# Kernel optimization log

Hardware: AMD Instinct MI355X
Metric: run time of the kernel (lower is better)

Reference implementation:

```python
import jax, jax.numpy as jnp
import numpy as np
import math

E = 1024   # embed_dim
H = 16     # num_heads
D = E // H # head_dim


def _rotary(x):
    # x: [B, H, S, D]. Faithful to the original quirky implementation:
    # pos_enc[:, 0::2] = sin(position * div_term), then cos/sin are taken OF that value.
    S = x.shape[2]
    position = jnp.arange(S, dtype=jnp.float32)[:, None]                     # [S,1]
    div_term = jnp.exp(jnp.arange(0, D, 2, dtype=jnp.float32) * (-math.log(10000.0) / D))  # [D/2]
    angle = jnp.sin(position * div_term)                                     # [S, D/2] == pos_enc[:,0::2]
    cos_t = jnp.cos(angle)                                                   # [S, D/2]
    sin_t = jnp.sin(angle)                                                   # [S, D/2]
    xe = x[..., 0::2]
    xo = x[..., 1::2]
    re = xe * cos_t - xo * sin_t
    ro = xo * cos_t + xe * sin_t
    # interleave even/odd back: [..., D/2, 2] -> [..., D]
    return jnp.stack([re, ro], axis=-1).reshape(x.shape)


def setup_inputs() -> dict:
    key = jax.random.key(0)
    ks = jax.random.split(key, 12)
    B, S = 4, 1024
    scale = 1.0 / math.sqrt(E)
    inp = {
        "query": jax.random.normal(ks[0], (B, S, E), dtype=jnp.float32),
        "key":   jax.random.normal(ks[1], (B, S, E), dtype=jnp.float32),
        "value": jax.random.normal(ks[2], (B, S, E), dtype=jnp.float32),
        # Linear params stored as [in, out]; y = x @ W + b
        "Wq": jax.random.normal(ks[3], (E, E), dtype=jnp.float32) * scale,
        "bq": jnp.zeros((E,), dtype=jnp.float32),
        "Wk": jax.random.normal(ks[4], (E, E), dtype=jnp.float32) * scale,
        "bk": jnp.zeros((E,), dtype=jnp.float32),
        "Wv": jax.random.normal(ks[5], (E, E), dtype=jnp.float32) * scale,
        "bv": jnp.zeros((E,), dtype=jnp.float32),
        "Wo": jax.random.normal(ks[6], (E, E), dtype=jnp.float32) * scale,
        "bo": jnp.zeros((E,), dtype=jnp.float32),
    }
    return inp


def reference(query, key, value, Wq, bq, Wk, bk, Wv, bv, Wo, bo):
    B, S, _ = query.shape
    # projections -> [B, H, S, D]
    q = (query @ Wq + bq).reshape(B, S, H, D).transpose(0, 2, 1, 3)
    k = (key   @ Wk + bk).reshape(B, S, H, D).transpose(0, 2, 1, 3)
    v = (value @ Wv + bv).reshape(B, S, H, D).transpose(0, 2, 1, 3)
    q = _rotary(q)
    k = _rotary(k)
    scores = jnp.einsum('bhsd,bhtd->bhst', q, k) / (D ** 0.5)  # [B,H,S,S]
    probs = jax.nn.softmax(scores, axis=-1)
    # dropout p=0 (eval) -> identity
    ctx = jnp.einsum('bhst,bhtd->bhsd', probs, v)              # [B,H,S,D]
    ctx = ctx.transpose(0, 2, 1, 3).reshape(B, S, E)
    out = ctx @ Wo + bo
    return out, probs
```

## Files before the change

kernel.cpp:

```cpp
#include <hip/hip_runtime.h>
#include <hip/hip_bf16.h>

typedef __attribute__((ext_vector_type(8))) short bf16x8;
typedef __attribute__((ext_vector_type(4))) float f32x4;
typedef unsigned short u16;

__device__ __forceinline__ u16 f2bf(float f) {
  unsigned u = __float_as_uint(f);
  u += 0x7fffu + ((u >> 16) & 1u);
  return (u16)(u >> 16);
}

__device__ __forceinline__ void gload16(const void* g, void* l) {
  __builtin_amdgcn_global_load_lds(
      (const __attribute__((address_space(1))) unsigned int*)g,
      (__attribute__((address_space(3))) unsigned int*)l, 16, 0, 0);
}

__device__ __forceinline__ void blockbar() {
  asm volatile("" ::: "memory");
  __builtin_amdgcn_s_barrier();
  asm volatile("" ::: "memory");
}

__global__ __launch_bounds__(256) void prep_kernel(
    const float* __restrict__ query, const float* __restrict__ key_,
    const float* __restrict__ value, u16* __restrict__ qin,
    u16* __restrict__ kin, u16* __restrict__ vin,
    const float* __restrict__ Wq, const float* __restrict__ Wk,
    const float* __restrict__ Wv, const float* __restrict__ Wo,
    u16* __restrict__ WqT, u16* __restrict__ WkT, u16* __restrict__ WvT,
    u16* __restrict__ WoT, float* __restrict__ cosT, float* __restrict__ sinT) {
  __shared__ float tile[32][33];
  const int z = blockIdx.z;
  const int bx = blockIdx.x;
  const int tid = threadIdx.x;
  if (z < 3) {
    const float* in = z == 0 ? query : z == 1 ? key_ : value;
    u16* out = z == 0 ? qin : z == 1 ? kin : vin;
    size_t i = ((size_t)bx * 256 + tid) * 4;
    float4 v = *(const float4*)(in + i);
    ushort4 o = make_ushort4(f2bf(v.x), f2bf(v.y), f2bf(v.z), f2bf(v.w));
    *(ushort4*)(out + i) = o;
  } else if (z == 3) {
    const int w = bx >> 10;
    const float* W = w == 0 ? Wq : w == 1 ? Wk : w == 2 ? Wv : Wo;
    u16* Wt = w == 0 ? WqT : w == 1 ? WkT : w == 2 ? WvT : WoT;
    int tx = tid & 31, ty = tid >> 5;
    int k0 = ((bx >> 5) & 31) * 32, n0 = (bx & 31) * 32;
#pragma unroll
    for (int i = 0; i < 4; ++i)
      tile[ty + i * 8][tx] = W[(size_t)(k0 + ty + i * 8) * 1024 + n0 + tx];
    __syncthreads();
#pragma unroll
    for (int i = 0; i < 4; ++i)
      Wt[(size_t)(n0 + ty + i * 8) * 1024 + k0 + tx] = f2bf(tile[tx][ty + i * 8]);
  } else {
    int i = bx * 256 + tid;
    if (i >= 1024 * 32) return;
    int s = i >> 5, p = i & 31;
    double freq = exp(-9.210340371976184 * (double)(2 * p) / 64.0);
    double ang = sin((double)s * freq);
    cosT[i] = (float)cos(ang);
    sinT[i] = (float)sin(ang);
  }
}

__global__ __launch_bounds__(256) void proj_gemm_kernel(
    const u16* __restrict__ qin, const u16* __restrict__ kin,
    const u16* __restrict__ vin, const u16* __restrict__ WqT,
    const u16* __restrict__ WkT, const u16* __restrict__ WvT,
    const float* __restrict__ bq, const float* __restrict__ bk,
    const float* __restrict__ bv, u16* __restrict__ qr, u16* __restrict__ kr,
    u16* __restrict__ vt, const float* __restrict__ cosT,
    const float* __restrict__ sinT) {
  __shared__ u16 lA[2][128 * 32];
  __shared__ u16 lB[2][128 * 32];
  const int z = blockIdx.z;
  const u16* A = z == 0 ? qin : z == 1 ? kin : vin;
  const u16* Bt = z == 0 ? WqT : z == 1 ? WkT : WvT;
  const float* bias = z == 0 ? bq : z == 1 ? bk : bv;

  const int tid = threadIdx.x;
  const int lane = tid & 63, wid = tid >> 6;
  const int wm = wid >> 1, wn = wid & 1;
  const int lr = lane & 15, kg = lane >> 4;
  const int m0 = blockIdx.y * 128, n0 = blockIdx.x * 128;

  auto stage = [&](int bu, int k0) {
#pragma unroll
    for (int it = 0; it < 2; ++it) {
      int o = tid * 16 + it * 4096;
      int row = o >> 6;
      int cbs = (((o >> 4) & 3) ^ (row & 3)) << 4;
      gload16((const char*)A + ((size_t)(m0 + row) * 1024 + k0) * 2 + cbs,
              (char*)lA[bu] + o);
      gload16((const char*)Bt + ((size_t)(n0 + row) * 1024 + k0) * 2 + cbs,
              (char*)lB[bu] + o);
    }
  };

  stage(0, 0);
  f32x4 acc[4][4] = {};
  for (int t = 0; t < 32; ++t) {
    if (t < 31) {
      stage((t + 1) & 1, (t + 1) * 32);
      asm volatile("s_waitcnt vmcnt(4)" ::: "memory");
    } else {
      asm volatile("s_waitcnt vmcnt(0)" ::: "memory");
    }
    blockbar();
    const int cb = t & 1;
    bf16x8 av[4], bv_[4];
#pragma unroll
    for (int i = 0; i < 4; ++i) {
      int ra = wm * 64 + i * 16 + lr;
      av[i] = *(const bf16x8*)((const char*)lA[cb] + ra * 64 + ((kg ^ (ra & 3)) << 4));
      int rb = wn * 64 + i * 16 + lr;
      bv_[i] = *(const bf16x8*)((const char*)lB[cb] + rb * 64 + ((kg ^ (rb & 3)) << 4));
    }
#pragma unroll
    for (int i = 0; i < 4; ++i)
#pragma unroll
      for (int j = 0; j < 4; ++j)
        acc[i][j] = __builtin_amdgcn_mfma_f32_16x16x32_bf16(av[i], bv_[j], acc[i][j], 0, 0, 0);
    blockbar();
  }

  if (z == 2) {
    const int bb = m0 >> 10;
#pragma unroll
    for (int i = 0; i < 4; ++i) {
      int srow = (m0 & 1023) + wm * 64 + i * 16 + kg * 4;
#pragma unroll
      for (int j = 0; j < 4; ++j) {
        int col = n0 + wn * 64 + j * 16 + lr;
        float bcol = bias[col];
        int h = col >> 6, d = col & 63;
        ushort4 o;
        o.x = f2bf(acc[i][j][0] + bcol);
        o.y = f2bf(acc[i][j][1] + bcol);
        o.z = f2bf(acc[i][j][2] + bcol);
        o.w = f2bf(acc[i][j][3] + bcol);
        *(ushort4*)(vt + ((size_t)((bb * 16 + h) * 64 + d)) * 1024 + srow) = o;
      }
    }
  } else {
    u16* Cout = z == 0 ? qr : kr;
#pragma unroll
    for (int i = 0; i < 4; ++i) {
#pragma unroll
      for (int j = 0; j < 4; ++j) {
        int col = n0 + wn * 64 + j * 16 + lr;
        float bcol = bias[col];
#pragma unroll
        for (int r = 0; r < 4; ++r) {
          int row = m0 + wm * 64 + i * 16 + kg * 4 + r;
          float v = acc[i][j][r] + bcol;
          float pv = __shfl_xor(v, 1);
          int p = (col & 63) >> 1;
          int s = row & 1023;
          float ct = cosT[s * 32 + p], st = sinT[s * 32 + p];
          float ov = (col & 1) ? (v * ct + pv * st) : (v * ct - pv * st);
          Cout[(size_t)row * 1024 + col] = f2bf(ov);
        }
      }
    }
  }
}

__global__ __launch_bounds__(256) void out_gemm_kernel(
    const u16* __restrict__ A, const u16* __restrict__ Bt,
    const float* __restrict__ bias, float* __restrict__ Cout) {
  __shared__ u16 lA[2][128 * 32];
  __shared__ u16 lB[2][128 * 32];
  const int tid = threadIdx.x;
  const int lane = tid & 63, wid = tid >> 6;
  const int wm = wid >> 1, wn = wid & 1;
  const int lr = lane & 15, kg = lane >> 4;
  const int m0 = blockIdx.y * 128, n0 = blockIdx.x * 128;

  auto stage = [&](int bu, int k0) {
#pragma unroll
    for (int it = 0; it < 2; ++it) {
      int o = tid * 16 + it * 4096;
      int row = o >> 6;
      int cbs = (((o >> 4) & 3) ^ (row & 3)) << 4;
      gload16((const char*)A + ((size_t)(m0 + row) * 1024 + k0) * 2 + cbs,
              (char*)lA[bu] + o);
      gload16((const char*)Bt + ((size_t)(n0 + row) * 1024 + k0) * 2 + cbs,
              (char*)lB[bu] + o);
    }
  };

  stage(0, 0);
  f32x4 acc[4][4] = {};
  for (int t = 0; t < 32; ++t) {
    if (t < 31) {
      stage((t + 1) & 1, (t + 1) * 32);
      asm volatile("s_waitcnt vmcnt(4)" ::: "memory");
    } else {
      asm volatile("s_waitcnt vmcnt(0)" ::: "memory");
    }
    blockbar();
    const int cb = t & 1;
    bf16x8 av[4], bv_[4];
#pragma unroll
    for (int i = 0; i < 4; ++i) {
      int ra = wm * 64 + i * 16 + lr;
      av[i] = *(const bf16x8*)((const char*)lA[cb] + ra * 64 + ((kg ^ (ra & 3)) << 4));
      int rb = wn * 64 + i * 16 + lr;
      bv_[i] = *(const bf16x8*)((const char*)lB[cb] + rb * 64 + ((kg ^ (rb & 3)) << 4));
    }
#pragma unroll
    for (int i = 0; i < 4; ++i)
#pragma unroll
      for (int j = 0; j < 4; ++j)
        acc[i][j] = __builtin_amdgcn_mfma_f32_16x16x32_bf16(av[i], bv_[j], acc[i][j], 0, 0, 0);
    blockbar();
  }
#pragma unroll
  for (int i = 0; i < 4; ++i)
#pragma unroll
    for (int j = 0; j < 4; ++j) {
      int col = n0 + wn * 64 + j * 16 + lr;
      float bcol = bias[col];
#pragma unroll
      for (int r = 0; r < 4; ++r) {
        int row = m0 + wm * 64 + i * 16 + kg * 4 + r;
        Cout[(size_t)row * 1024 + col] = acc[i][j][r] + bcol;
      }
    }
}

__global__ __launch_bounds__(256, 2) void fused_attn_kernel(
    const u16* __restrict__ qr, const u16* __restrict__ kr,
    const u16* __restrict__ vt, float* __restrict__ probs,
    u16* __restrict__ ctx) {
  __shared__ u16 lQ[32 * 64];
  __shared__ u16 lK[2][128 * 64];
  __shared__ u16 lV[2][64 * 128];
  __shared__ u16 lP[32 * 128];
  __shared__ float redM[4][32];
  __shared__ float redS[4][32];

  const int tid = threadIdx.x;
  const int lane = tid & 63, wid = tid >> 6;
  const int lr = lane & 15, kg = lane >> 4;
  const int z = blockIdx.y, b = z >> 4, h = z & 15;
  const int m0 = blockIdx.x * 32;

  const char* Qb = (const char*)qr + ((size_t)(b * 1024 + m0) * 1024 + h * 64) * 2;
  const char* Kb = (const char*)kr + ((size_t)(b * 1024) * 1024 + h * 64) * 2;
  const char* Vb = (const char*)vt + (size_t)z * 64 * 1024 * 2;

  auto stageK = [&](int bu, int c) {
#pragma unroll
    for (int it = 0; it < 4; ++it) {
      int o = tid * 16 + it * 4096;
      int row = o >> 7, ch = (o >> 4) & 7;
      gload16(Kb + (size_t)(c * 128 + row) * 2048 + ((ch ^ (row & 7)) << 4),
              (char*)lK[bu] + o);
    }
  };
  auto stageV = [&](int bu, int c) {
#pragma unroll
    for (int it = 0; it < 4; ++it) {
      int o = tid * 16 + it * 4096;
      int row = o >> 8, ch = (o >> 4) & 15;
      gload16(Vb + (size_t)row * 2048 + c * 256 + ((ch ^ (row & 15)) << 4),
              (char*)lV[bu] + o);
    }
  };

  {
    int o = tid * 16;
    int row = o >> 7, ch = (o >> 4) & 7;
    gload16(Qb + (size_t)row * 2048 + ((ch ^ (row & 7)) << 4), (char*)lQ + o);
  }
  stageK(0, 0);

  bf16x8 qf[2][2];
  f32x4 accS[8][2][2] = {};
#pragma unroll
  for (int c = 0; c < 8; ++c) {
    if (c < 7) {
      stageK((c + 1) & 1, c + 1);
      asm volatile("s_waitcnt vmcnt(4)" ::: "memory");
    } else {
      asm volatile("s_waitcnt vmcnt(0)" ::: "memory");
    }
    blockbar();
    if (c == 0) {
#pragma unroll
      for (int ii = 0; ii < 2; ++ii)
#pragma unroll
        for (int ks = 0; ks < 2; ++ks) {
          int ra = ii * 16 + lr;
          int cc = ks * 4 + kg;
          qf[ii][ks] = *(const bf16x8*)((const char*)lQ + ra * 128 + ((cc ^ (ra & 7)) << 4));
        }
    }
#pragma unroll
    for (int ks = 0; ks < 2; ++ks) {
      bf16x8 bvf[2];
#pragma unroll
      for (int jj = 0; jj < 2; ++jj) {
        int rb = wid * 32 + jj * 16 + lr;
        int cc = ks * 4 + kg;
        bvf[jj] = *(const bf16x8*)((const char*)lK[c & 1] + rb * 128 + ((cc ^ (rb & 7)) << 4));
      }
#pragma unroll
      for (int ii = 0; ii < 2; ++ii)
#pragma unroll
        for (int jj = 0; jj < 2; ++jj)
          accS[c][ii][jj] =
              __builtin_amdgcn_mfma_f32_16x16x32_bf16(qf[ii][ks], bvf[jj], accS[c][ii][jj], 0, 0, 0);
    }
    blockbar();
  }

  stageV(0, 0);

  float rmax[2][4];
#pragma unroll
  for (int ii = 0; ii < 2; ++ii)
#pragma unroll
    for (int r = 0; r < 4; ++r) rmax[ii][r] = -1e30f;
#pragma unroll
  for (int c = 0; c < 8; ++c)
#pragma unroll
    for (int ii = 0; ii < 2; ++ii)
#pragma unroll
      for (int jj = 0; jj < 2; ++jj)
#pragma unroll
        for (int r = 0; r < 4; ++r) {
          float v = accS[c][ii][jj][r] * 0.125f;
          accS[c][ii][jj][r] = v;
          rmax[ii][r] = fmaxf(rmax[ii][r], v);
        }
#pragma unroll
  for (int ii = 0; ii < 2; ++ii)
#pragma unroll
    for (int r = 0; r < 4; ++r) {
      float v = rmax[ii][r];
      v = fmaxf(v, __shfl_xor(v, 1));
      v = fmaxf(v, __shfl_xor(v, 2));
      v = fmaxf(v, __shfl_xor(v, 4));
      v = fmaxf(v, __shfl_xor(v, 8));
      rmax[ii][r] = v;
    }
  if (lr == 0) {
#pragma unroll
    for (int ii = 0; ii < 2; ++ii)
#pragma unroll
      for (int r = 0; r < 4; ++r) redM[wid][ii * 16 + kg * 4 + r] = rmax[ii][r];
  }
  asm volatile("s_waitcnt lgkmcnt(0)" ::: "memory");
  blockbar();
  float rowm[2][4], rsum[2][4];
#pragma unroll
  for (int ii = 0; ii < 2; ++ii)
#pragma unroll
    for (int r = 0; r < 4; ++r) {
      int row = ii * 16 + kg * 4 + r;
      rowm[ii][r] = fmaxf(fmaxf(redM[0][row], redM[1][row]), fmaxf(redM[2][row], redM[3][row]));
      rsum[ii][r] = 0.f;
    }
#pragma unroll
  for (int c = 0; c < 8; ++c)
#pragma unroll
    for (int ii = 0; ii < 2; ++ii)
#pragma unroll
      for (int jj = 0; jj < 2; ++jj)
#pragma unroll
        for (int r = 0; r < 4; ++r) {
          float e = __expf(accS[c][ii][jj][r] - rowm[ii][r]);
          accS[c][ii][jj][r] = e;
          rsum[ii][r] += e;
        }
#pragma unroll
  for (int ii = 0; ii < 2; ++ii)
#pragma unroll
    for (int r = 0; r < 4; ++r) {
      float v = rsum[ii][r];
      v += __shfl_xor(v, 1);
      v += __shfl_xor(v, 2);
      v += __shfl_xor(v, 4);
      v += __shfl_xor(v, 8);
      rsum[ii][r] = v;
    }
  if (lr == 0) {
#pragma unroll
    for (int ii = 0; ii < 2; ++ii)
#pragma unroll
      for (int r = 0; r < 4; ++r) redS[wid][ii * 16 + kg * 4 + r] = rsum[ii][r];
  }
  asm volatile("s_waitcnt lgkmcnt(0)" ::: "memory");
  blockbar();
  float inv[2][4];
#pragma unroll
  for (int ii = 0; ii < 2; ++ii)
#pragma unroll
    for (int r = 0; r < 4; ++r) {
      int row = ii * 16 + kg * 4 + r;
      inv[ii][r] = 1.0f / (redS[0][row] + redS[1][row] + redS[2][row] + redS[3][row]);
    }

  const int ipv = wid >> 1, jpv = wid & 1;
  f32x4 accPV[2] = {};
  float* Pg = probs + (size_t)z * 1024 * 1024 + (size_t)m0 * 1024;

#pragma unroll
  for (int c = 0; c < 8; ++c) {
    if (c < 7) stageV((c + 1) & 1, c + 1);
#pragma unroll
    for (int ii = 0; ii < 2; ++ii)
#pragma unroll
      for (int jj = 0; jj < 2; ++jj)
#pragma unroll
        for (int r = 0; r < 4; ++r) {
          float p = accS[c][ii][jj][r] * inv[ii][r];
          int row = ii * 16 + kg * 4 + r;
          int col = wid * 32 + jj * 16 + lr;
          Pg[(size_t)row * 1024 + c * 128 + col] = p;
          *(u16*)((char*)lP + row * 256 + ((((col >> 3) ^ (row & 15))) << 4) + (col & 7) * 2) =
              f2bf(p);
        }
    if (c < 7)
      asm volatile("s_waitcnt vmcnt(20) lgkmcnt(0)" ::: "memory");
    else
      asm volatile("s_waitcnt vmcnt(16) lgkmcnt(0)" ::: "memory");
    blockbar();
#pragma unroll
    for (int ks = 0; ks < 4; ++ks) {
      int cc = ks * 4 + kg;
      int ra = ipv * 16 + lr;
      bf16x8 pa = *(const bf16x8*)((const char*)lP + ra * 256 + ((cc ^ (ra & 15)) << 4));
#pragma unroll
      for (int jjj = 0; jjj < 2; ++jjj) {
        int rb = jpv * 32 + jjj * 16 + lr;
        bf16x8 vbf = *(const bf16x8*)((const char*)lV[c & 1] + rb * 256 + ((cc ^ (rb & 15)) << 4));
        accPV[jjj] = __builtin_amdgcn_mfma_f32_16x16x32_bf16(pa, vbf, accPV[jjj], 0, 0, 0);
      }
    }
    blockbar();
  }

#pragma unroll
  for (int jjj = 0; jjj < 2; ++jjj)
#pragma unroll
    for (int r = 0; r < 4; ++r) {
      int row = m0 + ipv * 16 + kg * 4 + r;
      int d = jpv * 32 + jjj * 16 + lr;
      ctx[((size_t)(b * 1024 + row)) * 1024 + h * 64 + d] = f2bf(accPV[jjj][r]);
    }
}

extern "C" void kernel_launch(void* const* d_in, const int* in_sizes, int n_in,
                              void* d_out, int out_size, void* d_ws, size_t ws_size,
                              hipStream_t stream) {
  const float* query = (const float*)d_in[0];
  const float* key_ = (const float*)d_in[1];
  const float* value = (const float*)d_in[2];
  const float* Wq = (const float*)d_in[3];
  const float* bq = (const float*)d_in[4];
  const float* Wk = (const float*)d_in[5];
  const float* bk = (const float*)d_in[6];
  const float* Wv = (const float*)d_in[7];
  const float* bv = (const float*)d_in[8];
  const float* Wo = (const float*)d_in[9];
  const float* bo = (const float*)d_in[10];

  float* out = (float*)d_out;
  float* probs = out + (size_t)4 * 1024 * 1024;

  char* w = (char*)d_ws;
  const size_t SZ_MK = (size_t)4096 * 1024 * 2;
  const size_t SZ_W = (size_t)1024 * 1024 * 2;
  u16* qin = (u16*)w; w += SZ_MK;
  u16* kin = (u16*)w; w += SZ_MK;
  u16* vin = (u16*)w; w += SZ_MK;
  u16* qr = (u16*)w; w += SZ_MK;
  u16* kr = (u16*)w; w += SZ_MK;
  u16* vt = (u16*)w; w += SZ_MK;
  u16* WqT = (u16*)w; w += SZ_W;
  u16* WkT = (u16*)w; w += SZ_W;
  u16* WvT = (u16*)w; w += SZ_W;
  u16* WoT = (u16*)w; w += SZ_W;
  float* cosT = (float*)w; w += 1024 * 32 * 4;
  float* sinT = (float*)w; w += 1024 * 32 * 4;
  u16* ctx = qin;

  dim3 blk(256);
  hipLaunchKernelGGL(prep_kernel, dim3(4096, 1, 5), blk, 0, stream,
                     query, key_, value, qin, kin, vin, Wq, Wk, Wv, Wo,
                     WqT, WkT, WvT, WoT, cosT, sinT);
  hipLaunchKernelGGL(proj_gemm_kernel, dim3(8, 32, 3), blk, 0, stream,
                     qin, kin, vin, WqT, WkT, WvT, bq, bk, bv, qr, kr, vt,
                     cosT, sinT);
  hipLaunchKernelGGL(fused_attn_kernel, dim3(32, 64), blk, 0, stream,
                     qr, kr, vt, probs, ctx);
  hipLaunchKernelGGL(out_gemm_kernel, dim3(8, 32), blk, 0, stream,
                     ctx, WoT, bo, out);
}
```

Baseline: 189.1 us.

## Recompute QK^T in two-pass softmax to cut registers and LDS for occupancy

The attention kernel no longer keeps all 8 score chunks in registers. A first pass computes QK^T only to accumulate exp row sums. A second pass over 64-column chunks recomputes the scores, normalises them, writes probs as float4, and does P·V, with K and V staged together in a shared double buffer. Max subtraction is dropped and operands are swapped so each lane holds contiguous columns. Together with the smaller LDS footprint, this lets launch bounds rise to 4 blocks per CU, at the cost of doing the QK^T MFMAs twice and risking exp overflow when score magnitudes are large.

```diff
diff --git a/kernel.cpp b/kernel.cpp
--- a/kernel.cpp
+++ b/kernel.cpp
@@ -233,15 +233,12 @@
     }
 }
 
-__global__ __launch_bounds__(256, 2) void fused_attn_kernel(
+__global__ __launch_bounds__(256, 4) void fused_attn_kernel(
     const u16* __restrict__ qr, const u16* __restrict__ kr,
     const u16* __restrict__ vt, float* __restrict__ probs,
     u16* __restrict__ ctx) {
-  __shared__ u16 lQ[32 * 64];
-  __shared__ u16 lK[2][128 * 64];
-  __shared__ u16 lV[2][64 * 128];
-  __shared__ u16 lP[32 * 128];
-  __shared__ float redM[4][32];
+  __shared__ u16 big[2][8192];
+  __shared__ u16 lP[32 * 64];
   __shared__ float redS[4][32];
 
   const int tid = threadIdx.x;
@@ -254,196 +251,148 @@
   const char* Kb = (const char*)kr + ((size_t)(b * 1024) * 1024 + h * 64) * 2;
   const char* Vb = (const char*)vt + (size_t)z * 64 * 1024 * 2;
 
-  auto stageK = [&](int bu, int c) {
+  bf16x8 qf[2][2];
+#pragma unroll
+  for (int ii = 0; ii < 2; ++ii)
+#pragma unroll
+    for (int ks = 0; ks < 2; ++ks)
+      qf[ii][ks] =
+          *(const bf16x8*)(Qb + (size_t)(ii * 16 + lr) * 2048 + (ks * 4 + kg) * 16);
+
+  auto stage1 = [&](int bu, int c) {
 #pragma unroll
     for (int it = 0; it < 4; ++it) {
       int o = tid * 16 + it * 4096;
       int row = o >> 7, ch = (o >> 4) & 7;
       gload16(Kb + (size_t)(c * 128 + row) * 2048 + ((ch ^ (row & 7)) << 4),
-              (char*)lK[bu] + o);
+              (char*)big[bu] + o);
     }
   };
-  auto stageV = [&](int bu, int c) {
-#pragma unroll
-    for (int it = 0; it < 4; ++it) {
+  auto stage2 = [&](int bu, int c2) {
+#pragma unroll
+    for (int it = 0; it < 2; ++it) {
       int o = tid * 16 + it * 4096;
-      int row = o >> 8, ch = (o >> 4) & 15;
-      gload16(Vb + (size_t)row * 2048 + c * 256 + ((ch ^ (row & 15)) << 4),
-              (char*)lV[bu] + o);
+      int row = o >> 7, ch = (o >> 4) & 7;
+      gload16(Kb + (size_t)(c2 * 64 + row) * 2048 + ((ch ^ (row & 7)) << 4),
+              (char*)big[bu] + o);
+    }
+#pragma unroll
+    for (int it = 0; it < 2; ++it) {
+      int o = tid * 16 + it * 4096;
+      int row = o >> 7, ch = (o >> 4) & 7;
+      gload16(Vb + (size_t)row * 2048 + c2 * 128 + ((ch ^ (row & 7)) << 4),
+              (char*)big[bu] + 8192 + o);
     }
   };
 
-  {
-    int o = tid * 16;
-    int row = o >> 7, ch = (o >> 4) & 7;
-    gload16(Qb + (size_t)row * 2048 + ((ch ^ (row & 7)) << 4), (char*)lQ + o);
-  }
-  stageK(0, 0);
-
-  bf16x8 qf[2][2];
-  f32x4 accS[8][2][2] = {};
-#pragma unroll
+  float rsum[2] = {0.f, 0.f};
+  stage1(0, 0);
+#pragma unroll 2
   for (int c = 0; c < 8; ++c) {
     if (c < 7) {
-      stageK((c + 1) & 1, c + 1);
+      stage1((c + 1) & 1, c + 1);
       asm volatile("s_waitcnt vmcnt(4)" ::: "memory");
     } else {
       asm volatile("s_waitcnt vmcnt(0)" ::: "memory");
     }
     blockbar();
-    if (c == 0) {
-#pragma unroll
-      for (int ii = 0; ii < 2; ++ii)
-#pragma unroll
-        for (int ks = 0; ks < 2; ++ks) {
-          int ra = ii * 16 + lr;
-          int cc = ks * 4 + kg;
-          qf[ii][ks] = *(const bf16x8*)((const char*)lQ + ra * 128 + ((cc ^ (ra & 7)) << 4));
-        }
-    }
+    const char* KB = (const char*)big[c & 1];
+    f32x4 aS[2][2] = {};
 #pragma unroll
     for (int ks = 0; ks < 2; ++ks) {
-      bf16x8 bvf[2];
+      bf16x8 kf[2];
 #pragma unroll
       for (int jj = 0; jj < 2; ++jj) {
         int rb = wid * 32 + jj * 16 + lr;
-        int cc = ks * 4 + kg;
-        bvf[jj] = *(const bf16x8*)((const char*)lK[c & 1] + rb * 128 + ((cc ^ (rb & 7)) << 4));
+        kf[jj] = *(const bf16x8*)(KB + rb * 128 + (((ks * 4 + kg) ^ (rb & 7)) << 4));
       }
 #pragma unroll
       for (int ii = 0; ii < 2; ++ii)
 #pragma unroll
         for (int jj = 0; jj < 2; ++jj)
-          accS[c][ii][jj] =
-              __builtin_amdgcn_mfma_f32_16x16x32_bf16(qf[ii][ks], bvf[jj], accS[c][ii][jj], 0, 0, 0);
-    }
-    blockbar();
-  }
-
-  stageV(0, 0);
-
-  float rmax[2][4];
-#pragma unroll
-  for (int ii = 0; ii < 2; ++ii)
-#pragma unroll
-    for (int r = 0; r < 4; ++r) rmax[ii][r] = -1e30f;
-#pragma unroll
-  for (int c = 0; c < 8; ++c)
+          aS[ii][jj] =
+              __builtin_amdgcn_mfma_f32_16x16x32_bf16(kf[jj], qf[ii][ks], aS[ii][jj], 0, 0, 0);
+    }
 #pragma unroll
     for (int ii = 0; ii < 2; ++ii)
 #pragma unroll
       for (int jj = 0; jj < 2; ++jj)
 #pragma unroll
-        for (int r = 0; r < 4; ++r) {
-          float v = accS[c][ii][jj][r] * 0.125f;
-          accS[c][ii][jj][r] = v;
-          rmax[ii][r] = fmaxf(rmax[ii][r], v);
-        }
-#pragma unroll
-  for (int ii = 0; ii < 2; ++ii)
-#pragma unroll
-    for (int r = 0; r < 4; ++r) {
-      float v = rmax[ii][r];
-      v = fmaxf(v, __shfl_xor(v, 1));
-      v = fmaxf(v, __shfl_xor(v, 2));
-      v = fmaxf(v, __shfl_xor(v, 4));
-      v = fmaxf(v, __shfl_xor(v, 8));
-      rmax[ii][r] = v;
-    }
-  if (lr == 0) {
-#pragma unroll
-    for (int ii = 0; ii < 2; ++ii)
-#pragma unroll
-      for (int r = 0; r < 4; ++r) redM[wid][ii * 16 + kg * 4 + r] = rmax[ii][r];
-  }
-  asm volatile("s_waitcnt lgkmcnt(0)" ::: "memory");
+        for (int r = 0; r < 4; ++r)
+          rsum[ii] += __expf(aS[ii][jj][r] * 0.125f);
+    blockbar();
+  }
+
+  stage2(0, 0);
+
+#pragma unroll
+  for (int ii = 0; ii < 2; ++ii) {
+    float v = rsum[ii];
+    v += __shfl_xor(v, 16);
+    v += __shfl_xor(v, 32);
+    rsum[ii] = v;
+  }
+  if (lane < 16) {
+    redS[wid][lane] = rsum[0];
+    redS[wid][16 + lane] = rsum[1];
+  }
+  asm volatile("s_waitcnt vmcnt(0) lgkmcnt(0)" ::: "memory");
   blockbar();
-  float rowm[2][4], rsum[2][4];
-#pragma unroll
-  for (int ii = 0; ii < 2; ++ii)
-#pragma unroll
-    for (int r = 0; r < 4; ++r) {
-      int row = ii * 16 + kg * 4 + r;
-      rowm[ii][r] = fmaxf(fmaxf(redM[0][row], redM[1][row]), fmaxf(redM[2][row], redM[3][row]));
-      rsum[ii][r] = 0.f;
-    }
-#pragma unroll
-  for (int c = 0; c < 8; ++c)
-#pragma unroll
-    for (int ii = 0; ii < 2; ++ii)
-#pragma unroll
-      for (int jj = 0; jj < 2; ++jj)
-#pragma unroll
-        for (int r = 0; r < 4; ++r) {
-          float e = __expf(accS[c][ii][jj][r] - rowm[ii][r]);
-          accS[c][ii][jj][r] = e;
-          rsum[ii][r] += e;
-        }
-#pragma unroll
-  for (int ii = 0; ii < 2; ++ii)
-#pragma unroll
-    for (int r = 0; r < 4; ++r) {
-      float v = rsum[ii][r];
-      v += __shfl_xor(v, 1);
-      v += __shfl_xor(v, 2);
-      v += __shfl_xor(v, 4);
-      v += __shfl_xor(v, 8);
-      rsum[ii][r] = v;
-    }
-  if (lr == 0) {
-#pragma unroll
-    for (int ii = 0; ii < 2; ++ii)
-#pragma unroll
-      for (int r = 0; r < 4; ++r) redS[wid][ii * 16 + kg * 4 + r] = rsum[ii][r];
-  }
-  asm volatile("s_waitcnt lgkmcnt(0)" ::: "memory");
-  blockbar();
-  float inv[2][4];
-#pragma unroll
-  for (int ii = 0; ii < 2; ++ii)
-#pragma unroll
-    for (int r = 0; r < 4; ++r) {
-      int row = ii * 16 + kg * 4 + r;
-      inv[ii][r] = 1.0f / (redS[0][row] + redS[1][row] + redS[2][row] + redS[3][row]);
-    }
+  float inv[2];
+#pragma unroll
+  for (int ii = 0; ii < 2; ++ii) {
+    int row = ii * 16 + lr;
+    inv[ii] = 1.0f / (redS[0][row] + redS[1][row] + redS[2][row] + redS[3][row]);
+  }
 
   const int ipv = wid >> 1, jpv = wid & 1;
   f32x4 accPV[2] = {};
   float* Pg = probs + (size_t)z * 1024 * 1024 + (size_t)m0 * 1024;
 
-#pragma unroll
-  for (int c = 0; c < 8; ++c) {
-    if (c < 7) stageV((c + 1) & 1, c + 1);
-#pragma unroll
-    for (int ii = 0; ii < 2; ++ii)
-#pragma unroll
-      for (int jj = 0; jj < 2; ++jj)
-#pragma unroll
-        for (int r = 0; r < 4; ++r) {
-          float p = accS[c][ii][jj][r] * inv[ii][r];
-          int row = ii * 16 + kg * 4 + r;
-          int col = wid * 32 + jj * 16 + lr;
-          Pg[(size_t)row * 1024 + c * 128 + col] = p;
-          *(u16*)((char*)lP + row * 256 + ((((col >> 3) ^ (row & 15))) << 4) + (col & 7) * 2) =
-              f2bf(p);
-        }
-    if (c < 7)
-      asm volatile("s_waitcnt vmcnt(20) lgkmcnt(0)" ::: "memory");
-    else
-      asm volatile("s_waitcnt vmcnt(16) lgkmcnt(0)" ::: "memory");
-    blockbar();
-#pragma unroll
-    for (int ks = 0; ks < 4; ++ks) {
-      int cc = ks * 4 + kg;
+#pragma unroll 2
+  for (int c2 = 0; c2 < 16; ++c2) {
+    const int cur = c2 & 1;
+    if (c2 < 15) stage2(cur ^ 1, c2 + 1);
+    const char* KB = (const char*)big[cur];
+    f32x4 aS2[2] = {};
+#pragma unroll
+    for (int ks = 0; ks < 2; ++ks) {
+      int rb = wid * 16 + lr;
+      bf16x8 kf = *(const bf16x8*)(KB + rb * 128 + (((ks * 4 + kg) ^ (rb & 7)) << 4));
+#pragma unroll
+      for (int ii = 0; ii < 2; ++ii)
+        aS2[ii] = __builtin_amdgcn_mfma_f32_16x16x32_bf16(kf, qf[ii][ks], aS2[ii], 0, 0, 0);
+    }
+#pragma unroll
+    for (int ii = 0; ii < 2; ++ii) {
+      float4 p4;
+      p4.x = __expf(aS2[ii][0] * 0.125f) * inv[ii];
+      p4.y = __expf(aS2[ii][1] * 0.125f) * inv[ii];
+      p4.z = __expf(aS2[ii][2] * 0.125f) * inv[ii];
+      p4.w = __expf(aS2[ii][3] * 0.125f) * inv[ii];
+      int row = ii * 16 + lr;
+      *(float4*)(Pg + (size_t)row * 1024 + c2 * 64 + wid * 16 + kg * 4) = p4;
+      int bytecol = (wid * 16 + kg * 4) * 2;
+      int ch = bytecol >> 4, sub = bytecol & 15;
+      ushort4 pb = make_ushort4(f2bf(p4.x), f2bf(p4.y), f2bf(p4.z), f2bf(p4.w));
+      *(ushort4*)((char*)lP + row * 128 + ((ch ^ (row & 7)) << 4) + sub) = pb;
+    }
+    asm volatile("s_waitcnt lgkmcnt(0)" ::: "memory");
+    blockbar();
+    const char* VB = (const char*)big[cur] + 8192;
+#pragma unroll
+    for (int ks = 0; ks < 2; ++ks) {
       int ra = ipv * 16 + lr;
-      bf16x8 pa = *(const bf16x8*)((const char*)lP + ra * 256 + ((cc ^ (ra & 15)) << 4));
+      bf16x8 pa =
+          *(const bf16x8*)((const char*)lP + ra * 128 + (((ks * 4 + kg) ^ (ra & 7)) << 4));
 #pragma unroll
       for (int jjj = 0; jjj < 2; ++jjj) {
         int rb = jpv * 32 + jjj * 16 + lr;
-        bf16x8 vbf = *(const bf16x8*)((const char*)lV[c & 1] + rb * 256 + ((cc ^ (rb & 15)) << 4));
+        bf16x8 vbf = *(const bf16x8*)(VB + rb * 128 + (((ks * 4 + kg) ^ (rb & 7)) << 4));
         accPV[jjj] = __builtin_amdgcn_mfma_f32_16x16x32_bf16(pa, vbf, accPV[jjj], 0, 0, 0);
       }
     }
+    if (c2 < 15) asm volatile("s_waitcnt vmcnt(2)" ::: "memory");
     blockbar();
   }
 
```

New measurement: 197.3 us. 4.3% more time.

## Split fused attention work across eight waves per block

Applied to the files above, without the earlier changes.

Raises the fused attention block from 256 to 512 threads. Each wave now owns 16 key columns instead of 32 in QK^T and a single 16x16 output tile in PV, which halves the per-thread score accumulator registers. Staging loads, waitcnt thresholds and the cross-wave max/sum reductions are rescaled for eight waves. The aim is more waves in flight to hide latency, at the cost of more barrier participants and less fragment reuse per wave.

```diff
diff --git a/kernel.cpp b/kernel.cpp
--- a/kernel.cpp
+++ b/kernel.cpp
@@ -233,7 +233,7 @@
     }
 }
 
-__global__ __launch_bounds__(256, 2) void fused_attn_kernel(
+__global__ __launch_bounds__(512, 4) void fused_attn_kernel(
     const u16* __restrict__ qr, const u16* __restrict__ kr,
     const u16* __restrict__ vt, float* __restrict__ probs,
     u16* __restrict__ ctx) {
@@ -241,8 +241,8 @@
   __shared__ u16 lK[2][128 * 64];
   __shared__ u16 lV[2][64 * 128];
   __shared__ u16 lP[32 * 128];
-  __shared__ float redM[4][32];
-  __shared__ float redS[4][32];
+  __shared__ float redM[8][32];
+  __shared__ float redS[8][32];
 
   const int tid = threadIdx.x;
   const int lane = tid & 63, wid = tid >> 6;
@@ -256,8 +256,8 @@
 
   auto stageK = [&](int bu, int c) {
 #pragma unroll
-    for (int it = 0; it < 4; ++it) {
-      int o = tid * 16 + it * 4096;
+    for (int it = 0; it < 2; ++it) {
+      int o = tid * 16 + it * 8192;
       int row = o >> 7, ch = (o >> 4) & 7;
       gload16(Kb + (size_t)(c * 128 + row) * 2048 + ((ch ^ (row & 7)) << 4),
               (char*)lK[bu] + o);
@@ -265,15 +265,15 @@
   };
   auto stageV = [&](int bu, int c) {
 #pragma unroll
-    for (int it = 0; it < 4; ++it) {
-      int o = tid * 16 + it * 4096;
+    for (int it = 0; it < 2; ++it) {
+      int o = tid * 16 + it * 8192;
       int row = o >> 8, ch = (o >> 4) & 15;
       gload16(Vb + (size_t)row * 2048 + c * 256 + ((ch ^ (row & 15)) << 4),
               (char*)lV[bu] + o);
     }
   };
 
-  {
+  if (tid < 256) {
     int o = tid * 16;
     int row = o >> 7, ch = (o >> 4) & 7;
     gload16(Qb + (size_t)row * 2048 + ((ch ^ (row & 7)) << 4), (char*)lQ + o);
@@ -281,12 +281,12 @@
   stageK(0, 0);
 
   bf16x8 qf[2][2];
-  f32x4 accS[8][2][2] = {};
+  f32x4 accS[8][2] = {};
 #pragma unroll
   for (int c = 0; c < 8; ++c) {
     if (c < 7) {
       stageK((c + 1) & 1, c + 1);
-      asm volatile("s_waitcnt vmcnt(4)" ::: "memory");
+      asm volatile("s_waitcnt vmcnt(2)" ::: "memory");
     } else {
       asm volatile("s_waitcnt vmcnt(0)" ::: "memory");
     }
@@ -303,19 +303,13 @@
     }
 #pragma unroll
     for (int ks = 0; ks < 2; ++ks) {
-      bf16x8 bvf[2];
-#pragma unroll
-      for (int jj = 0; jj < 2; ++jj) {
-        int rb = wid * 32 + jj * 16 + lr;
-        int cc = ks * 4 + kg;
-        bvf[jj] = *(const bf16x8*)((const char*)lK[c & 1] + rb * 128 + ((cc ^ (rb & 7)) << 4));
-      }
+      int rb = wid * 16 + lr;
+      bf16x8 kf =
+          *(const bf16x8*)((const char*)lK[c & 1] + rb * 128 + (((ks * 4 + kg) ^ (rb & 7)) << 4));
 #pragma unroll
       for (int ii = 0; ii < 2; ++ii)
-#pragma unroll
-        for (int jj = 0; jj < 2; ++jj)
-          accS[c][ii][jj] =
-              __builtin_amdgcn_mfma_f32_16x16x32_bf16(qf[ii][ks], bvf[jj], accS[c][ii][jj], 0, 0, 0);
+        accS[c][ii] =
+            __builtin_amdgcn_mfma_f32_16x16x32_bf16(qf[ii][ks], kf, accS[c][ii], 0, 0, 0);
     }
     blockbar();
   }
@@ -332,13 +326,11 @@
 #pragma unroll
     for (int ii = 0; ii < 2; ++ii)
 #pragma unroll
-      for (int jj = 0; jj < 2; ++jj)
-#pragma unroll
-        for (int r = 0; r < 4; ++r) {
-          float v = accS[c][ii][jj][r] * 0.125f;
-          accS[c][ii][jj][r] = v;
-          rmax[ii][r] = fmaxf(rmax[ii][r], v);
-        }
+      for (int r = 0; r < 4; ++r) {
+        float v = accS[c][ii][r] * 0.125f;
+        accS[c][ii][r] = v;
+        rmax[ii][r] = fmaxf(rmax[ii][r], v);
+      }
 #pragma unroll
   for (int ii = 0; ii < 2; ++ii)
 #pragma unroll
@@ -364,7 +356,11 @@
 #pragma unroll
     for (int r = 0; r < 4; ++r) {
       int row = ii * 16 + kg * 4 + r;
-      rowm[ii][r] = fmaxf(fmaxf(redM[0][row], redM[1][row]), fmaxf(redM[2][row], redM[3][row]));
+      float m01 = fmaxf(redM[0][row], redM[1][row]);
+      float m23 = fmaxf(redM[2][row], redM[3][row]);
+      float m45 = fmaxf(redM[4][row], redM[5][row]);
+      float m67 = fmaxf(redM[6][row], redM[7][row]);
+      rowm[ii][r] = fmaxf(fmaxf(m01, m23), fmaxf(m45, m67));
       rsum[ii][r] = 0.f;
     }
 #pragma unroll
@@ -372,13 +368,11 @@
 #pragma unroll
     for (int ii = 0; ii < 2; ++ii)
 #pragma unroll
-      for (int jj = 0; jj < 2; ++jj)
-#pragma unroll
-        for (int r = 0; r < 4; ++r) {
-          float e = __expf(accS[c][ii][jj][r] - rowm[ii][r]);
-          accS[c][ii][jj][r] = e;
-          rsum[ii][r] += e;
-        }
+      for (int r = 0; r < 4; ++r) {
+        float e = __expf(accS[c][ii][r] - rowm[ii][r]);
+        accS[c][ii][r] = e;
+        rsum[ii][r] += e;
+      }
 #pragma unroll
   for (int ii = 0; ii < 2; ++ii)
 #pragma unroll
@@ -404,11 +398,13 @@
 #pragma unroll
     for (int r = 0; r < 4; ++r) {
       int row = ii * 16 + kg * 4 + r;
-      inv[ii][r] = 1.0f / (redS[0][row] + redS[1][row] + redS[2][row] + redS[3][row]);
-    }
-
-  const int ipv = wid >> 1, jpv = wid & 1;
-  f32x4 accPV[2] = {};
+      float s = redS[0][row] + redS[1][row] + redS[2][row] + redS[3][row] +
+                redS[4][row] + redS[5][row] + redS[6][row] + redS[7][row];
+      inv[ii][r] = 1.0f / s;
+    }
+
+  const int ipv = wid >> 2, jpv = wid & 3;
+  f32x4 accPV = {};
   float* Pg = probs + (size_t)z * 1024 * 1024 + (size_t)m0 * 1024;
 
 #pragma unroll
@@ -417,44 +413,37 @@
 #pragma unroll
     for (int ii = 0; ii < 2; ++ii)
 #pragma unroll
-      for (int jj = 0; jj < 2; ++jj)
-#pragma unroll
-        for (int r = 0; r < 4; ++r) {
-          float p = accS[c][ii][jj][r] * inv[ii][r];
-          int row = ii * 16 + kg * 4 + r;
-          int col = wid * 32 + jj * 16 + lr;
-          Pg[(size_t)row * 1024 + c * 128 + col] = p;
-          *(u16*)((char*)lP + row * 256 + ((((col >> 3) ^ (row & 15))) << 4) + (col & 7) * 2) =
-              f2bf(p);
-        }
+      for (int r = 0; r < 4; ++r) {
+        float p = accS[c][ii][r] * inv[ii][r];
+        int row = ii * 16 + kg * 4 + r;
+        int col = wid * 16 + lr;
+        Pg[(size_t)row * 1024 + c * 128 + col] = p;
+        *(u16*)((char*)lP + row * 256 + ((((col >> 3) ^ (row & 15))) << 4) + (col & 7) * 2) =
+            f2bf(p);
+      }
     if (c < 7)
-      asm volatile("s_waitcnt vmcnt(20) lgkmcnt(0)" ::: "memory");
+      asm volatile("s_waitcnt vmcnt(10) lgkmcnt(0)" ::: "memory");
     else
-      asm volatile("s_waitcnt vmcnt(16) lgkmcnt(0)" ::: "memory");
+      asm volatile("s_waitcnt vmcnt(8) lgkmcnt(0)" ::: "memory");
     blockbar();
 #pragma unroll
     for (int ks = 0; ks < 4; ++ks) {
       int cc = ks * 4 + kg;
       int ra = ipv * 16 + lr;
       bf16x8 pa = *(const bf16x8*)((const char*)lP + ra * 256 + ((cc ^ (ra & 15)) << 4));
-#pragma unroll
-      for (int jjj = 0; jjj < 2; ++jjj) {
-        int rb = jpv * 32 + jjj * 16 + lr;
-        bf16x8 vbf = *(const bf16x8*)((const char*)lV[c & 1] + rb * 256 + ((cc ^ (rb & 15)) << 4));
-        accPV[jjj] = __builtin_amdgcn_mfma_f32_16x16x32_bf16(pa, vbf, accPV[jjj], 0, 0, 0);
-      }
-    }
-    blockbar();
-  }
-
-#pragma unroll
-  for (int jjj = 0; jjj < 2; ++jjj)
-#pragma unroll
-    for (int r = 0; r < 4; ++r) {
-      int row = m0 + ipv * 16 + kg * 4 + r;
-      int d = jpv * 32 + jjj * 16 + lr;
-      ctx[((size_t)(b * 1024 + row)) * 1024 + h * 64 + d] = f2bf(accPV[jjj][r]);
-    }
+      int rb = jpv * 16 + lr;
+      bf16x8 vbf = *(const bf16x8*)((const char*)lV[c & 1] + rb * 256 + ((cc ^ (rb & 15)) << 4));
+      accPV = __builtin_amdgcn_mfma_f32_16x16x32_bf16(pa, vbf, accPV, 0, 0, 0);
+    }
+    blockbar();
+  }
+
+#pragma unroll
+  for (int r = 0; r < 4; ++r) {
+    int row = m0 + ipv * 16 + kg * 4 + r;
+    int d = jpv * 16 + lr;
+    ctx[((size_t)(b * 1024 + row)) * 1024 + h * 64 + d] = f2bf(accPV[r]);
+  }
 }
 
 extern "C" void kernel_launch(void* const* d_in, const int* in_sizes, int n_in,
@@ -499,7 +488,7 @@
   hipLaunchKernelGGL(proj_gemm_kernel, dim3(8, 32, 3), blk, 0, stream,
                      qin, kin, vin, WqT, WkT, WvT, bq, bk, bv, qr, kr, vt,
                      cosT, sinT);
-  hipLaunchKernelGGL(fused_attn_kernel, dim3(32, 64), blk, 0, stream,
+  hipLaunchKernelGGL(fused_attn_kernel, dim3(32, 64), dim3(512), 0, stream,
                      qr, kr, vt, probs, ctx);
   hipLaunchKernelGGL(out_gemm_kernel, dim3(8, 32), blk, 0, stream,
                      ctx, WoT, bo, out);
```

Result: no change. 192.6 us (+1.8%).
